# Kernel tuning notes

Measured on AMD Instinct MI355X. Metric: run time of the kernel, lower is better.

## Reference

```python
import jax, jax.numpy as jnp
import numpy as np

D_MODEL, HIDDEN, N_EXPERTS, TOP_K = 1024, 2048, 8, 2
RMS_EPS = 1e-6


def setup_inputs() -> dict:
    key = jax.random.key(0)
    ks = jax.random.split(key, 6)
    B, S = 4, 2048
    return {
        "x": jax.random.normal(ks[0], (B, S, D_MODEL), jnp.float32),
        "norm_weight": jnp.ones((D_MODEL,), jnp.float32),
        "gate_w": jax.random.normal(ks[1], (N_EXPERTS, D_MODEL), jnp.float32) * 0.02,
        "w1": jax.random.normal(ks[2], (N_EXPERTS, HIDDEN, D_MODEL), jnp.float32) * 0.02,
        "b1": jnp.zeros((N_EXPERTS, HIDDEN), jnp.float32),
        "w2": jax.random.normal(ks[3], (N_EXPERTS, D_MODEL, HIDDEN), jnp.float32) * 0.02,
        "b2": jnp.zeros((N_EXPERTS, D_MODEL), jnp.float32),
    }


def reference(x, norm_weight, gate_w, w1, b1, w2, b2):
    B, S, D = x.shape
    E = gate_w.shape[0]
    # RMSNorm
    t = x * jax.lax.rsqrt(jnp.mean(x * x, axis=-1, keepdims=True) + RMS_EPS) * norm_weight
    tokens = t.reshape(-1, D)                      # [T, D]
    T = tokens.shape[0]
    # Top-k routing (eval mode: no gate noise)
    gate_logits = tokens @ gate_w.T                # [T, E]
    gate_scores, expert_idx = jax.lax.top_k(gate_logits, TOP_K)
    routing_weights = jax.nn.softmax(gate_scores, axis=-1)  # [T, K]
    # Per-token per-expert combine weight (scatter routing weights into [T, E])
    combine = jnp.zeros((T, E), tokens.dtype).at[
        jnp.arange(T)[:, None], expert_idx
    ].add(routing_weights)
    # Scan over experts; inactive tokens have combine weight 0, matching the
    # masked gather/scatter-add math of the original exactly.
    def body(acc, params):
        W1, B1, W2, B2, c = params                 # c: [T]
        h = jax.nn.gelu(tokens @ W1.T + B1, approximate=False)  # [T, H]
        o = h @ W2.T + B2                          # [T, D]
        return acc + c[:, None] * o, None

    out, _ = jax.lax.scan(body, jnp.zeros_like(tokens), (w1, b1, w2, b2, combine.T))
    return x + out.reshape(B, S, D)
```

## Files before the change

### kernel.cpp

```cpp
#include <hip/hip_runtime.h>
#include <hip/hip_bf16.h>
#include <stdint.h>

#define D_MODEL 1024
#define HIDDEN  2048
#define N_EXP   8
#define T_TOK   8192
#define BM      256
#define MAXPOS  (16384 + N_EXP * BM)
#define ROWT    (MAXPOS / BM)

typedef __attribute__((ext_vector_type(4))) float f32x4;
typedef __attribute__((ext_vector_type(8))) short short8v;

__device__ __forceinline__ unsigned short f2bf(float f) {
    union { float f; unsigned int u; } v; v.f = f;
    unsigned int u = v.u;
    unsigned int r = (u + 0x7fffu + ((u >> 16) & 1u)) >> 16;
    return (unsigned short)r;
}
__device__ __forceinline__ float bf2f(unsigned short s) {
    union { unsigned int u; float f; } v; v.u = ((unsigned int)s) << 16;
    return v.f;
}

__device__ __forceinline__ void gload_lds16(const void* g, void* l) {
    __builtin_amdgcn_global_load_lds(
        reinterpret_cast<const __attribute__((address_space(1))) unsigned int*>(
            reinterpret_cast<uintptr_t>(g)),
        reinterpret_cast<__attribute__((address_space(3))) unsigned int*>(
            (uint32_t)reinterpret_cast<uintptr_t>(l)),
        16, 0, 0);
}

__global__ void rms_gate_kernel(const float* __restrict__ x,
                                const float* __restrict__ nw,
                                const float* __restrict__ gw,
                                unsigned short* __restrict__ tb,
                                int* __restrict__ tok_e,
                                float* __restrict__ tok_w) {
    const int wave = threadIdx.x >> 6;
    const int lane = threadIdx.x & 63;
    const int t = blockIdx.x * 4 + wave;

    const float4* xr = (const float4*)(x + (size_t)t * D_MODEL);
    const float4* wr = (const float4*)nw;
    float4 xv[4], wv[4];
    #pragma unroll
    for (int j = 0; j < 4; j++) {
        xv[j] = xr[j * 64 + lane];
        wv[j] = wr[j * 64 + lane];
    }

    float ssq = 0.0f;
    #pragma unroll
    for (int j = 0; j < 4; j++)
        ssq += xv[j].x * xv[j].x + xv[j].y * xv[j].y + xv[j].z * xv[j].z + xv[j].w * xv[j].w;
    #pragma unroll
    for (int off = 32; off; off >>= 1) ssq += __shfl_xor(ssq, off);
    const float scale = rsqrtf(ssq * (1.0f / D_MODEL) + 1e-6f);

    float4 tn[4];
    #pragma unroll
    for (int j = 0; j < 4; j++) {
        tn[j].x = xv[j].x * wv[j].x * scale;
        tn[j].y = xv[j].y * wv[j].y * scale;
        tn[j].z = xv[j].z * wv[j].z * scale;
        tn[j].w = xv[j].w * wv[j].w * scale;
    }

    ushort4* tw = (ushort4*)(tb + (size_t)t * D_MODEL);
    #pragma unroll
    for (int j = 0; j < 4; j++) {
        ushort4 o;
        o.x = f2bf(tn[j].x); o.y = f2bf(tn[j].y);
        o.z = f2bf(tn[j].z); o.w = f2bf(tn[j].w);
        tw[j * 64 + lane] = o;
    }

    float d[8];
    #pragma unroll
    for (int e = 0; e < 8; e++) {
        d[e] = 0.0f;
        #pragma unroll
        for (int j = 0; j < 4; j++) {
            float4 g = ((const float4*)(gw + e * D_MODEL))[j * 64 + lane];
            d[e] += tn[j].x * g.x + tn[j].y * g.y + tn[j].z * g.z + tn[j].w * g.w;
        }
    }
    #pragma unroll
    for (int e = 0; e < 8; e++) {
        #pragma unroll
        for (int off = 32; off; off >>= 1) d[e] += __shfl_xor(d[e], off);
    }

    if (lane == 0) {
        int i0 = 0;
        #pragma unroll
        for (int e = 1; e < 8; e++) if (d[e] > d[i0]) i0 = e;
        int i1 = -1;
        #pragma unroll
        for (int e = 0; e < 8; e++)
            if (e != i0 && (i1 < 0 || d[e] > d[i1])) i1 = e;
        float e1 = expf(d[i1] - d[i0]);
        float w0 = 1.0f / (1.0f + e1);
        ((int2*)tok_e)[t]   = make_int2(i0, i1);
        ((float2*)tok_w)[t] = make_float2(w0, e1 * w0);
    }
}

__global__ void hist_kernel(const int* __restrict__ tok_e, int* __restrict__ counts) {
    __shared__ int lh[8];
    if (threadIdx.x < 8) lh[threadIdx.x] = 0;
    __syncthreads();
    int i = blockIdx.x * 512 + threadIdx.x;
    atomicAdd(&lh[tok_e[i]], 1);
    atomicAdd(&lh[tok_e[i + 256]], 1);
    __syncthreads();
    if (threadIdx.x < 8) atomicAdd(&counts[threadIdx.x], lh[threadIdx.x]);
}

__global__ void scan_fill_kernel(int* __restrict__ perm_tok,
                                 const int* __restrict__ counts,
                                 int* __restrict__ poff, int* __restrict__ pos_ctr) {
    int i = blockIdx.x * 256 + threadIdx.x;
    if (i < MAXPOS) perm_tok[i] = 0;
    if (blockIdx.x == 0 && threadIdx.x == 0) {
        int acc = 0; poff[0] = 0;
        #pragma unroll
        for (int e = 0; e < 8; e++) {
            pos_ctr[e] = 0;
            acc += (counts[e] + (BM - 1)) & ~(BM - 1);
            poff[e + 1] = acc;
        }
    }
}

__global__ void scatter_kernel(const int* __restrict__ tok_e,
                               const int* __restrict__ poff, int* __restrict__ pos_ctr,
                               int* __restrict__ perm_tok, int* __restrict__ tok_pos) {
    __shared__ int lh[8], lbase[8];
    if (threadIdx.x < 8) lh[threadIdx.x] = 0;
    __syncthreads();
    int t = blockIdx.x * 256 + threadIdx.x;
    int2 ee = ((const int2*)tok_e)[t];
    int p0 = atomicAdd(&lh[ee.x], 1);
    int p1 = atomicAdd(&lh[ee.y], 1);
    __syncthreads();
    if (threadIdx.x < 8) lbase[threadIdx.x] = atomicAdd(&pos_ctr[threadIdx.x], lh[threadIdx.x]);
    __syncthreads();
    int q0 = poff[ee.x] + lbase[ee.x] + p0;
    int q1 = poff[ee.y] + lbase[ee.y] + p1;
    perm_tok[q0] = t;
    perm_tok[q1] = t;
    ((int2*)tok_pos)[t] = make_int2(q0, q1);
}

__global__ void cvt_bf16_kernel(const float4* __restrict__ in,
                                ushort4* __restrict__ outp, int n4) {
    int i = blockIdx.x * blockDim.x + threadIdx.x;
    if (i >= n4) return;
    float4 v = in[i];
    ushort4 o; o.x = f2bf(v.x); o.y = f2bf(v.y); o.z = f2bf(v.z); o.w = f2bf(v.w);
    outp[i] = o;
}


#define STAGE_ALL(BUF, K0) do { \
    gload_lds16(gb[0][0] + (K0), lds + (BUF)*65536 + 32768 + (w*16)*128); \
    gload_lds16(gb[0][1] + (K0), lds + (BUF)*65536 + 32768 + (w*16 + 8)*128); \
    gload_lds16(gb[1][0] + (K0), lds + (BUF)*65536 + 32768 + (128 + w*16)*128); \
    gload_lds16(gb[1][1] + (K0), lds + (BUF)*65536 + 32768 + (128 + w*16 + 8)*128); \
    gload_lds16(ga[0] + (K0), lds + (BUF)*65536 + rsA[0]*128); \
    gload_lds16(ga[1] + (K0), lds + (BUF)*65536 + rsA[1]*128); \
    gload_lds16(ga[2] + (K0), lds + (BUF)*65536 + rsA[2]*128); \
    gload_lds16(ga[3] + (K0), lds + (BUF)*65536 + rsA[3]*128); \
} while (0)

template <int MODE, int K, int N>
__global__ __launch_bounds__(512) void moe_gemm_kernel(
        const unsigned short* __restrict__ A,
        const unsigned short* __restrict__ W,
        const float* __restrict__ bias,
        const int* __restrict__ perm_tok,
        const int* __restrict__ poff,
        unsigned short* __restrict__ Cout) {
    constexpr int NT  = N / 256;
    constexpr int K2  = K * 2;
    constexpr int NTK = K / 64;
    __shared__ __align__(16) char lds[131072];

    const int nwg = gridDim.x;
    const int cpx = nwg >> 3;
    const int bid = (int)blockIdx.x;
    const int swzb = (bid & 7) * cpx + (bid >> 3);
    const int rt = swzb / NT, nt = swzb % NT;
    const int row_base = rt * BM;
    if (row_base >= poff[8]) return;
    int e = 0;
    while (poff[e + 1] <= row_base) ++e;
    const int n0 = nt * 256;

    const int tid = threadIdx.x;
    const int w = tid >> 6, l = tid & 63;
    const int wr = w >> 2, wc = w & 3;
    const int cswz = ((l & 7) * 16) ^ (l & 32);

    const char* Ab = (const char*)A;
    const char* Wb = (const char*)W;
    const char* ga[4];
    const char* gb[2][2];
    int rsA[4];
    #pragma unroll
    for (int s = 0; s < 4; s++) {
        int rstart = (w < 4) ? (s * 32 + w * 8) : (128 + s * 32 + (w - 4) * 8);
        rsA[s] = rstart;
        int r = row_base + rstart + (l >> 3);
        size_t arow = (MODE == 1) ? (size_t)perm_tok[r] : (size_t)r;
        ga[s] = Ab + arow * K2 + cswz;
    }
    #pragma unroll
    for (int g = 0; g < 2; g++)
        #pragma unroll
        for (int j = 0; j < 2; j++) {
            int r = g * 128 + w * 16 + j * 8 + (l >> 3);
            gb[g][j] = Wb + ((size_t)e * N + n0 + r) * K2 + cswz;
        }

    const int aRow = (wr * 128 + (l & 15)) * 128;
    const int bRow = (wc * 64 + (l & 15)) * 128;
    const int csw0 = (((l >> 4) * 16)      ) ^ ((l & 4) << 3);
    const int csw1 = (64 + ((l >> 4) * 16) ) ^ ((l & 4) << 3);

    f32x4 acc[8][4];
    #pragma unroll
    for (int mi = 0; mi < 8; mi++)
        #pragma unroll
        for (int ni = 0; ni < 4; ni++) acc[mi][ni] = (f32x4)(0.0f);
    short8v bfr[4][2];

    STAGE_ALL(0, 0);
    __syncthreads();

    int cur = 0;
    #pragma unroll 1
    for (int t = 0; t < NTK; ++t) {
        if (t + 1 < NTK) {
            const int kn = (t + 1) * 128;
            STAGE_ALL(1 - cur, kn);
        }
        const char* BL = lds + cur * 65536 + 32768 + bRow;
        #pragma unroll
        for (int ni = 0; ni < 4; ni++) {
            bfr[ni][0] = *(const short8v*)(BL + ni * 2048 + csw0);
            bfr[ni][1] = *(const short8v*)(BL + ni * 2048 + csw1);
        }
        const char* AL = lds + cur * 65536 + aRow;
        #pragma unroll
        for (int q = 0; q < 4; q++) {
            short8v af0 = *(const short8v*)(AL + q * 4096 + csw0);
            short8v af1 = *(const short8v*)(AL + q * 4096 + csw1);
            short8v af2 = *(const short8v*)(AL + q * 4096 + 2048 + csw0);
            short8v af3 = *(const short8v*)(AL + q * 4096 + 2048 + csw1);
            #pragma unroll
            for (int ni = 0; ni < 4; ni++) {
                acc[2*q][ni]   = __builtin_amdgcn_mfma_f32_16x16x32_bf16(af0, bfr[ni][0], acc[2*q][ni],   0, 0, 0);
                acc[2*q][ni]   = __builtin_amdgcn_mfma_f32_16x16x32_bf16(af1, bfr[ni][1], acc[2*q][ni],   0, 0, 0);
                acc[2*q+1][ni] = __builtin_amdgcn_mfma_f32_16x16x32_bf16(af2, bfr[ni][0], acc[2*q+1][ni], 0, 0, 0);
                acc[2*q+1][ni] = __builtin_amdgcn_mfma_f32_16x16x32_bf16(af3, bfr[ni][1], acc[2*q+1][ni], 0, 0, 0);
            }
        }
        __syncthreads();
        cur ^= 1;
    }

    short* sl = (short*)lds;
    #pragma unroll
    for (int h = 0; h < 2; h++) {
        if ((wc >> 1) == h) {
            #pragma unroll
            for (int mi = 0; mi < 8; mi++) {
                #pragma unroll
                for (int ni = 0; ni < 4; ni++) {
                    int gcol = wc * 64 + ni * 16 + (l & 15);
                    int lc   = gcol - h * 128;
                    float bv = bias[e * N + n0 + gcol];
                    #pragma unroll
                    for (int j = 0; j < 4; j++) {
                        int lr = wr * 128 + mi * 16 + (l >> 4) * 4 + j;
                        float v = acc[mi][ni][j] + bv;
                        if (MODE == 1)
                            v = 0.5f * v * (1.0f + erff(v * 0.70710678118654752f));
                        sl[lr * 136 + lc] = (short)f2bf(v);
                    }
                }
            }
        }
        __syncthreads();
        {
            const int rr = tid >> 4;
            const int cc = tid & 15;
            #pragma unroll
            for (int p = 0; p < 8; p++) {
                int lr = p * 32 + rr;
                short8v v = *(const short8v*)&sl[lr * 136 + cc * 8];
                *(short8v*)(Cout + (size_t)(row_base + lr) * N + n0 + h * 128 + cc * 8) = v;
            }
        }
        __syncthreads();
    }
}

__global__ void combine_kernel(const float* __restrict__ x,
                               const int* __restrict__ tok_pos,
                               const float* __restrict__ tok_w,
                               const unsigned short* __restrict__ obuf,
                               float* __restrict__ out) {
    const int wave = threadIdx.x >> 6;
    const int lane = threadIdx.x & 63;
    const int t = blockIdx.x * 4 + wave;
    int2 pp = ((const int2*)tok_pos)[t];
    float2 ww = ((const float2*)tok_w)[t];
    const float4* xr = (const float4*)(x + (size_t)t * D_MODEL);
    float4* orow = (float4*)(out + (size_t)t * D_MODEL);
    const short4* o0 = (const short4*)(obuf + (size_t)pp.x * D_MODEL);
    const short4* o1 = (const short4*)(obuf + (size_t)pp.y * D_MODEL);
    #pragma unroll
    for (int j = 0; j < 4; j++) {
        int idx = j * 64 + lane;
        float4 xv = xr[idx];
        short4 a = o0[idx];
        short4 b = o1[idx];
        float4 r;
        r.x = xv.x + ww.x * bf2f((unsigned short)a.x) + ww.y * bf2f((unsigned short)b.x);
        r.y = xv.y + ww.x * bf2f((unsigned short)a.y) + ww.y * bf2f((unsigned short)b.y);
        r.z = xv.z + ww.x * bf2f((unsigned short)a.z) + ww.y * bf2f((unsigned short)b.z);
        r.w = xv.w + ww.x * bf2f((unsigned short)a.w) + ww.y * bf2f((unsigned short)b.w);
        orow[idx] = r;
    }
}

extern "C" void kernel_launch(void* const* d_in, const int* in_sizes, int n_in,
                              void* d_out, int out_size, void* d_ws, size_t ws_size,
                              hipStream_t stream) {
    const float* x  = (const float*)d_in[0];
    const float* nw = (const float*)d_in[1];
    const float* gw = (const float*)d_in[2];
    const float* w1 = (const float*)d_in[3];
    const float* b1 = (const float*)d_in[4];
    const float* w2 = (const float*)d_in[5];
    const float* b2 = (const float*)d_in[6];
    float* out = (float*)d_out;
    char* ws = (char*)d_ws;

    size_t off = 0;
    unsigned short* tb   = (unsigned short*)(ws + off); off += (size_t)T_TOK * D_MODEL * 2;
    unsigned short* w1b  = (unsigned short*)(ws + off); off += (size_t)N_EXP * HIDDEN * D_MODEL * 2;
    unsigned short* w2b  = (unsigned short*)(ws + off); off += (size_t)N_EXP * D_MODEL * HIDDEN * 2;
    unsigned short* h    = (unsigned short*)(ws + off); off += (size_t)MAXPOS * HIDDEN * 2;
    unsigned short* obuf = (unsigned short*)(ws + off); off += (size_t)MAXPOS * D_MODEL * 2;
    int*   perm_tok = (int*)(ws + off);   off += MAXPOS * 4;
    int*   tok_e    = (int*)(ws + off);   off += T_TOK * 2 * 4;
    float* tok_w    = (float*)(ws + off); off += T_TOK * 2 * 4;
    int*   tok_pos  = (int*)(ws + off);   off += T_TOK * 2 * 4;
    int*   meta     = (int*)(ws + off);
    int* counts  = meta;
    int* pos_ctr = meta + 8;
    int* poff    = meta + 16;

    hipMemsetAsync(meta, 0, 32, stream);

    rms_gate_kernel<<<T_TOK / 4, 256, 0, stream>>>(x, nw, gw, tb, tok_e, tok_w);

    const int n4 = N_EXP * HIDDEN * D_MODEL / 4;
    cvt_bf16_kernel<<<n4 / 256, 256, 0, stream>>>((const float4*)w1, (ushort4*)w1b, n4);
    cvt_bf16_kernel<<<n4 / 256, 256, 0, stream>>>((const float4*)w2, (ushort4*)w2b, n4);

    hist_kernel<<<32, 256, 0, stream>>>(tok_e, counts);
    scan_fill_kernel<<<MAXPOS / 256, 256, 0, stream>>>(perm_tok, counts, poff, pos_ctr);
    scatter_kernel<<<T_TOK / 256, 256, 0, stream>>>(tok_e, poff, pos_ctr, perm_tok, tok_pos);

    moe_gemm_kernel<1, D_MODEL, HIDDEN><<<ROWT * (HIDDEN / 256), 512, 0, stream>>>(
        tb, w1b, b1, perm_tok, poff, h);
    moe_gemm_kernel<2, HIDDEN, D_MODEL><<<ROWT * (D_MODEL / 256), 512, 0, stream>>>(
        h, w2b, b2, perm_tok, poff, obuf);

    combine_kernel<<<T_TOK / 4, 256, 0, stream>>>(x, tok_pos, tok_w, obuf, out);
}
```

Measured before the change: 381.8 us.

## Interleave global-to-LDS staging with MFMA phases using fine-grained waitcnt barriers

Splits each K-tile of the expert GEMM into four phases. Each phase issues a slice of the next tile's global-to-LDS loads, waits on a partial vmcnt, synchronises with raw s_barrier, and then runs its MFMA group at raised wave priority. The K loop is unrolled by two so the LDS buffer indices become compile-time constants. The aim is to overlap memory traffic with matrix math instead of issuing all loads up front and doing one full __syncthreads per tile. In exchange it adds more barriers per tile and depends on hand-tuned vmcnt counts being correct. The last iteration also issues a redundant prefetch of tile 0.

```diff
diff --git a/kernel.cpp b/kernel.cpp
--- a/kernel.cpp
+++ b/kernel.cpp
@@ -166,16 +166,50 @@
 }
 
 
-#define STAGE_ALL(BUF, K0) do { \
-    gload_lds16(gb[0][0] + (K0), lds + (BUF)*65536 + 32768 + (w*16)*128); \
-    gload_lds16(gb[0][1] + (K0), lds + (BUF)*65536 + 32768 + (w*16 + 8)*128); \
-    gload_lds16(gb[1][0] + (K0), lds + (BUF)*65536 + 32768 + (128 + w*16)*128); \
-    gload_lds16(gb[1][1] + (K0), lds + (BUF)*65536 + 32768 + (128 + w*16 + 8)*128); \
-    gload_lds16(ga[0] + (K0), lds + (BUF)*65536 + rsA[0]*128); \
-    gload_lds16(ga[1] + (K0), lds + (BUF)*65536 + rsA[1]*128); \
-    gload_lds16(ga[2] + (K0), lds + (BUF)*65536 + rsA[2]*128); \
-    gload_lds16(ga[3] + (K0), lds + (BUF)*65536 + rsA[3]*128); \
-} while (0)
+#define SB(G, BUF, K0) \
+    gload_lds16(gb[G][0] + (K0), lds + (BUF)*65536 + 32768 + ((G)*128 + w*16)*128); \
+    gload_lds16(gb[G][1] + (K0), lds + (BUF)*65536 + 32768 + ((G)*128 + w*16 + 8)*128);
+#define SA(S, BUF, K0) \
+    gload_lds16(ga[S]   + (K0), lds + (BUF)*65536 + rsA[S]*128); \
+    gload_lds16(ga[S+1] + (K0), lds + (BUF)*65536 + rsA[(S)+1]*128);
+
+#define PHASE(CUR, Q, STAGE_STMT, VM) \
+  { \
+    const char* AL_ = lds + (CUR)*65536 + aRow + (2*(Q))*2048; \
+    short8v af0 = *(const short8v*)(AL_ + csw0); \
+    short8v af1 = *(const short8v*)(AL_ + csw1); \
+    short8v af2 = *(const short8v*)(AL_ + 2048 + csw0); \
+    short8v af3 = *(const short8v*)(AL_ + 2048 + csw1); \
+    STAGE_STMT \
+    asm volatile("s_waitcnt vmcnt(" #VM ")" ::: "memory"); \
+    __builtin_amdgcn_s_barrier(); \
+    asm volatile("s_waitcnt lgkmcnt(0)" ::: "memory"); \
+    __builtin_amdgcn_sched_barrier(0); \
+    __builtin_amdgcn_s_setprio(1); \
+    _Pragma("unroll") \
+    for (int ni = 0; ni < 4; ni++) { \
+      acc[2*(Q)][ni]   = __builtin_amdgcn_mfma_f32_16x16x32_bf16(af0, bfr[ni][0], acc[2*(Q)][ni],   0,0,0); \
+      acc[2*(Q)][ni]   = __builtin_amdgcn_mfma_f32_16x16x32_bf16(af1, bfr[ni][1], acc[2*(Q)][ni],   0,0,0); \
+      acc[2*(Q)+1][ni] = __builtin_amdgcn_mfma_f32_16x16x32_bf16(af2, bfr[ni][0], acc[2*(Q)+1][ni], 0,0,0); \
+      acc[2*(Q)+1][ni] = __builtin_amdgcn_mfma_f32_16x16x32_bf16(af3, bfr[ni][1], acc[2*(Q)+1][ni], 0,0,0); \
+    } \
+    __builtin_amdgcn_s_setprio(0); \
+    __builtin_amdgcn_s_barrier(); \
+  }
+
+#define KTILE(CUR, KN) \
+  { \
+    const char* BL_ = lds + (CUR)*65536 + 32768 + bRow; \
+    _Pragma("unroll") \
+    for (int ni = 0; ni < 4; ni++) { \
+      bfr[ni][0] = *(const short8v*)(BL_ + ni*2048 + csw0); \
+      bfr[ni][1] = *(const short8v*)(BL_ + ni*2048 + csw1); \
+    } \
+    PHASE(CUR, 0, SB(0, 1-(CUR), KN), 4) \
+    PHASE(CUR, 1, SB(1, 1-(CUR), KN), 5) \
+    PHASE(CUR, 2, SA(0, 1-(CUR), KN), 6) \
+    PHASE(CUR, 3, SA(2, 1-(CUR), KN), 3) \
+  }
 
 template <int MODE, int K, int N>
 __global__ __launch_bounds__(512) void moe_gemm_kernel(
@@ -239,40 +273,18 @@
         for (int ni = 0; ni < 4; ni++) acc[mi][ni] = (f32x4)(0.0f);
     short8v bfr[4][2];
 
-    STAGE_ALL(0, 0);
-    __syncthreads();
-
-    int cur = 0;
-    #pragma unroll 1
-    for (int t = 0; t < NTK; ++t) {
-        if (t + 1 < NTK) {
-            const int kn = (t + 1) * 128;
-            STAGE_ALL(1 - cur, kn);
-        }
-        const char* BL = lds + cur * 65536 + 32768 + bRow;
-        #pragma unroll
-        for (int ni = 0; ni < 4; ni++) {
-            bfr[ni][0] = *(const short8v*)(BL + ni * 2048 + csw0);
-            bfr[ni][1] = *(const short8v*)(BL + ni * 2048 + csw1);
-        }
-        const char* AL = lds + cur * 65536 + aRow;
-        #pragma unroll
-        for (int q = 0; q < 4; q++) {
-            short8v af0 = *(const short8v*)(AL + q * 4096 + csw0);
-            short8v af1 = *(const short8v*)(AL + q * 4096 + csw1);
-            short8v af2 = *(const short8v*)(AL + q * 4096 + 2048 + csw0);
-            short8v af3 = *(const short8v*)(AL + q * 4096 + 2048 + csw1);
-            #pragma unroll
-            for (int ni = 0; ni < 4; ni++) {
-                acc[2*q][ni]   = __builtin_amdgcn_mfma_f32_16x16x32_bf16(af0, bfr[ni][0], acc[2*q][ni],   0, 0, 0);
-                acc[2*q][ni]   = __builtin_amdgcn_mfma_f32_16x16x32_bf16(af1, bfr[ni][1], acc[2*q][ni],   0, 0, 0);
-                acc[2*q+1][ni] = __builtin_amdgcn_mfma_f32_16x16x32_bf16(af2, bfr[ni][0], acc[2*q+1][ni], 0, 0, 0);
-                acc[2*q+1][ni] = __builtin_amdgcn_mfma_f32_16x16x32_bf16(af3, bfr[ni][1], acc[2*q+1][ni], 0, 0, 0);
-            }
-        }
-        __syncthreads();
-        cur ^= 1;
-    }
+    SB(0, 0, 0) SB(1, 0, 0) SA(0, 0, 0) SA(2, 0, 0)
+    asm volatile("s_waitcnt vmcnt(3)" ::: "memory");
+    __builtin_amdgcn_s_barrier();
+
+    for (int t = 0; t < NTK; t += 2) {
+        const int kn0 = (t + 1) * 128;
+        const int kn1 = (t + 2 < NTK ? t + 2 : 0) * 128;
+        KTILE(0, kn0)
+        KTILE(1, kn1)
+    }
+
+    __syncthreads();
 
     short* sl = (short*)lds;
     #pragma unroll
```

Result: slower. 399.6 us (+4.7%).
